# Performance work log

Measured on AMD Instinct MI355X. Metric: run time of the kernel, lower is better.

The kernel has to match this reference:

```python
import jax, jax.numpy as jnp
import numpy as np

K = 16  # neighbors

def _pdist2(a, b):
    # squared euclidean distances (B,N,M); same argsort order as torch.cdist
    return (jnp.sum(a * a, -1)[:, :, None] + jnp.sum(b * b, -1)[:, None, :]
            - 2.0 * jnp.einsum('bnd,bmd->bnm', a, b))

def _knn(xyz, k):
    d2 = jax.lax.stop_gradient(_pdist2(xyz, xyz))
    return jax.lax.top_k(-d2, k)[1]  # (B,N,k) smallest distances

_gather_f = jax.vmap(lambda f, i: f[:, i])  # feat (C,N), idx (...,) -> (C,...)
_gather_x = jax.vmap(lambda x, i: x[i])     # xyz (N,D), idx (...,) -> (...,D)

def _bn_act(x, g, b):
    # eval-mode BatchNorm (running_mean=0, running_var=1) folded to affine, + LeakyReLU(0.1)
    shp = (1, -1) + (1,) * (x.ndim - 2)
    return jax.nn.leaky_relu(x * g.reshape(shp) + b.reshape(shp), 0.1)

def _lfa(xyz, feat, idx, Wm, gm, bm, Ws, Wp, gp, bp):
    # xyz (B,N,3), feat (B,C,N), idx (B,N,K)
    neigh_feat = _gather_f(feat, idx)          # (B,C,N,K)
    neigh_xyz = _gather_x(xyz, idx)            # (B,N,K,3)
    center = xyz[:, :, None, :]
    diff = center - neigh_xyz
    dist = jnp.linalg.norm(diff, axis=-1, keepdims=True)
    rel = jnp.concatenate([diff, dist, jnp.broadcast_to(center, neigh_xyz.shape), neigh_xyz], axis=-1)
    rel = jnp.transpose(rel, (0, 3, 1, 2))     # (B,10,N,K)
    x = jnp.concatenate([neigh_feat, rel], axis=1)          # (B,C+10,N,K)
    x = _bn_act(jnp.einsum('oc,bcnk->bonk', Wm, x), gm, bm)  # (B,O,N,K)
    a = jax.nn.softmax(jnp.einsum('oc,bcnk->bonk', Ws, x), axis=3)
    x = jnp.sum(x * a, axis=3)                               # attentive pool over K -> (B,O,N)
    return _bn_act(jnp.einsum('oc,bcn->bon', Wp, x), gp, bp)

def _interp(src_xyz, src_feat, tgt_xyz):
    nn_idx = jnp.argmin(jax.lax.stop_gradient(_pdist2(tgt_xyz, src_xyz)), axis=-1)  # (B,N)
    return _gather_f(src_feat, nn_idx)  # (B,C,N)


def setup_inputs() -> dict:
    key = jax.random.key(0)
    ks = jax.random.split(key, 24)
    B, N, CIN, NC = 2, 8192, 6, 13
    M1, M2 = N // 2, N // 4
    w = lambda i, shp: jax.random.normal(ks[i], shp, jnp.float32) * 0.05
    ones = lambda c: jnp.ones((c,), jnp.float32)
    zeros = lambda c: jnp.zeros((c,), jnp.float32)
    inp = {
        'xyz': jax.random.uniform(ks[0], (B, N, 3), jnp.float32),
        'feat': jax.random.normal(ks[1], (B, N, CIN), jnp.float32),
        'sel1': jax.random.randint(ks[2], (B, M1), 0, N),
        'sel2': jax.random.randint(ks[3], (B, M2), 0, M1),
        'Wpre': w(4, (64, CIN)), 'gpre': ones(64), 'bpre': zeros(64),
        'W1m': w(5, (64, 74)), 'g1m': ones(64), 'b1m': zeros(64),
        'W1s': w(6, (64, 64)), 'W1p': w(7, (64, 64)), 'g1p': ones(64), 'b1p': zeros(64),
        'W2m': w(8, (128, 74)), 'g2m': ones(128), 'b2m': zeros(128),
        'W2s': w(9, (128, 128)), 'W2p': w(10, (128, 128)), 'g2p': ones(128), 'b2p': zeros(128),
        'W3m': w(11, (256, 138)), 'g3m': ones(256), 'b3m': zeros(256),
        'W3s': w(12, (256, 256)), 'W3p': w(13, (256, 256)), 'g3p': ones(256), 'b3p': zeros(256),
        'Wu2': w(14, (128, 384)), 'gu2': ones(128), 'bu2': zeros(128),
        'Wu1': w(15, (64, 192)), 'gu1': ones(64), 'bu1': zeros(64),
        'Wh1': w(16, (64, 64)), 'bh1': zeros(64),
        'Wh2': w(17, (NC, 64)), 'bh2': zeros(NC),
    }
    return inp


def reference(xyz, feat, sel1, sel2, Wpre, gpre, bpre,
              W1m, g1m, b1m, W1s, W1p, g1p, b1p,
              W2m, g2m, b2m, W2s, W2p, g2p, b2p,
              W3m, g3m, b3m, W3s, W3p, g3p, b3p,
              Wu2, gu2, bu2, Wu1, gu1, bu1,
              Wh1, bh1, Wh2, bh2):
    ft = jnp.transpose(feat, (0, 2, 1))                       # (B,Cin,N)
    x0 = _bn_act(jnp.einsum('oc,bcn->bon', Wpre, ft), gpre, bpre)
    n0 = _knn(xyz, K)
    x1 = _lfa(xyz, x0, n0, W1m, g1m, b1m, W1s, W1p, g1p, b1p)  # (B,64,N)
    xyz1 = _gather_x(xyz, sel1); f1 = _gather_f(x1, sel1)      # random downsample 0.5
    n1 = _knn(xyz1, K)
    x2 = _lfa(xyz1, f1, n1, W2m, g2m, b2m, W2s, W2p, g2p, b2p)  # (B,128,M1)
    xyz2 = _gather_x(xyz1, sel2); f2 = _gather_f(x2, sel2)
    n2 = _knn(xyz2, K)
    x3 = _lfa(xyz2, f2, n2, W3m, g3m, b3m, W3s, W3p, g3p, b3p)  # (B,256,M2)
    up2 = _interp(xyz2, x3, xyz1)
    d2 = _bn_act(jnp.einsum('oc,bcn->bon', Wu2, jnp.concatenate([up2, x2], 1)), gu2, bu2)
    up1 = _interp(xyz1, d2, xyz)
    d1 = _bn_act(jnp.einsum('oc,bcn->bon', Wu1, jnp.concatenate([up1, x1], 1)), gu1, bu1)
    h = jax.nn.leaky_relu(jnp.einsum('oc,bcn->bon', Wh1, d1) + bh1[None, :, None], 0.1)
    logits = jnp.einsum('oc,bcn->bon', Wh2, h) + bh2[None, :, None]
    return jnp.transpose(logits, (0, 2, 1))                    # (B,N,num_classes)
```

## Files before the change

kernel.cpp:

```cpp
#include <hip/hip_runtime.h>
#include <hip/hip_bf16.h>

#pragma clang fp contract(off)

typedef unsigned long long ull;

__device__ __forceinline__ float lrelu(float v) { return v >= 0.0f ? v : 0.1f * v; }

__device__ __forceinline__ float sumsq3(float x, float y, float z) {
    return ((x * x) + (y * y)) + (z * z);
}

__device__ __forceinline__ float dot3fma(float ax, float ay, float az,
                                         float bx, float by, float bz) {
    float d = ax * bx;
    d = __builtin_fmaf(ay, by, d);
    d = __builtin_fmaf(az, bz, d);
    return d;
}

__device__ __forceinline__ float distf(float qn, float sn, float dot) {
    float s = qn + sn;
    return __builtin_fmaf(-2.0f, dot, s);
}

__device__ __forceinline__ ull packkey(float d, int i) {
    unsigned u = __float_as_uint(d);
    u = (u & 0x80000000u) ? ~u : (u | 0x80000000u);
    return ((ull)u << 32) | (unsigned)i;
}

__device__ __forceinline__ ull shfl_xor_u64(ull v, int mask) {
    int lo = __shfl_xor((int)(v & 0xffffffffull), mask);
    int hi = __shfl_xor((int)(v >> 32), mask);
    return ((ull)(unsigned)hi << 32) | (unsigned)lo;
}

__device__ __forceinline__ void cswap64(ull& x, ull& y) {
    bool sw = y < x;
    ull lo = sw ? y : x;
    ull hi = sw ? x : y;
    x = lo; y = hi;
}

__device__ __forceinline__ ull min64(ull a, ull b) { return a < b ? a : b; }

__global__ void k_pre(const float* __restrict__ feat, const float* __restrict__ W,
                      const float* __restrict__ g, const float* __restrict__ bb,
                      float* __restrict__ x0) {
    int p = blockIdx.x * blockDim.x + threadIdx.x;
    if (p >= 2 * 8192) return;
    const float* f = feat + (size_t)p * 6;
    float fv[6];
#pragma unroll
    for (int c = 0; c < 6; ++c) fv[c] = f[c];
    float* out = x0 + (size_t)p * 64;
    for (int o = 0; o < 64; ++o) {
        float s = 0.0f;
#pragma unroll
        for (int c = 0; c < 6; ++c) s = __builtin_fmaf(W[o * 6 + c], fv[c], s);
        float v = s * g[o];
        v = v + bb[o];
        out[o] = lrelu(v);
    }
}

__global__ void k_wt(const float* __restrict__ W, float* __restrict__ WT, int M, int K) {
    int i = blockIdx.x * 256 + threadIdx.x;
    if (i >= M * K) return;
    int o = i / K, c = i - o * K;
    WT[c * M + o] = W[i];
}

template <int LPQ, int TS>
__launch_bounds__(256)
__global__ void k_knn_reg(const float* __restrict__ xyz, int* __restrict__ out_idx, int Npts) {
    constexpr int QPB = 256 / LPQ;
    __shared__ float4 sp[TS];
    int b = blockIdx.y;
    int tid = threadIdx.x;
    int qi = tid / LPQ;
    int l = tid % LPQ;
    int q = blockIdx.x * QPB + qi;
    const float* X = xyz + (size_t)b * Npts * 3;
    float qx = X[q * 3], qy = X[q * 3 + 1], qz = X[q * 3 + 2];
    float qn = sumsq3(qx, qy, qz);

    ull key[16];
#pragma unroll
    for (int u = 0; u < 16; ++u) key[u] = ~0ull;
    ull p0 = ~0ull, p1 = ~0ull, p2 = ~0ull, p3 = ~0ull;
    int cnt = 0;
    float tau_d = INFINITY;

    auto merge = [&]() {
        cswap64(p0, p2); cswap64(p1, p3); cswap64(p0, p1);
        cswap64(p2, p3); cswap64(p1, p2);
        key[12] = min64(key[12], p3);
        key[13] = min64(key[13], p2);
        key[14] = min64(key[14], p1);
        key[15] = min64(key[15], p0);
#pragma unroll
        for (int dstep = 8; dstep >= 1; dstep >>= 1) {
#pragma unroll
            for (int i = 0; i < 16; ++i) {
                if (!(i & dstep)) cswap64(key[i], key[i + dstep]);
            }
        }
        p0 = p1 = p2 = p3 = ~0ull;
        cnt = 0;
        ull t = key[15];
#pragma unroll
        for (int mask = 1; mask < LPQ; mask <<= 1) t = min64(t, shfl_xor_u64(t, mask));
        unsigned hu = (unsigned)(t >> 32);
        unsigned fb = (hu & 0x80000000u) ? (hu & 0x7fffffffu) : ~hu;
        tau_d = (hu == 0xffffffffu) ? INFINITY : __uint_as_float(fb);
    };

    for (int t0 = 0; t0 < Npts; t0 += TS) {
        __syncthreads();
        for (int j = tid; j < TS; j += 256) {
            int i = t0 + j;
            float px = X[i * 3], py = X[i * 3 + 1], pz = X[i * 3 + 2];
            sp[j] = make_float4(px, py, pz, sumsq3(px, py, pz));
        }
        __syncthreads();
        for (int j = l; j < TS; j += LPQ) {
            float4 p = sp[j];
            float d = distf(qn, p.w, dot3fma(qx, qy, qz, p.x, p.y, p.z));
            if (d <= tau_d) {
                p3 = p2; p2 = p1; p1 = p0;
                p0 = packkey(d, t0 + j);
                ++cnt;
            }
            if (__any(cnt >= 4)) merge();
        }
    }
    if (__any(cnt > 0)) merge();

    for (int mask = 1; mask < LPQ; mask <<= 1) {
        ull ok[16];
#pragma unroll
        for (int i = 0; i < 16; ++i) ok[i] = shfl_xor_u64(key[15 - i], mask);
#pragma unroll
        for (int i = 0; i < 16; ++i) key[i] = min64(ok[i], key[i]);
#pragma unroll
        for (int dstep = 8; dstep >= 1; dstep >>= 1) {
#pragma unroll
            for (int i = 0; i < 16; ++i) {
                if (!(i & dstep)) cswap64(key[i], key[i + dstep]);
            }
        }
    }

    if (l == 0) {
        int* o = out_idx + ((size_t)b * Npts + q) * 16;
#pragma unroll
        for (int u = 0; u < 16; ++u) o[u] = (int)(unsigned)(key[u] & 0xffffffffull);
    }
}

template <int C>
__global__ void k_gather(const float* __restrict__ src_xyz, const float* __restrict__ src_feat,
                         const int* __restrict__ sel, float* __restrict__ dst_xyz,
                         float* __restrict__ dst_feat, int M, int Nsrc) {
    int b = blockIdx.y, m = blockIdx.x;
    int s = sel[(size_t)b * M + m];
    const float* fx = src_xyz + ((size_t)b * Nsrc + s) * 3;
    const float* ff = src_feat + ((size_t)b * Nsrc + s) * C;
    float* dx = dst_xyz + ((size_t)b * M + m) * 3;
    float* df = dst_feat + ((size_t)b * M + m) * C;
    if (threadIdx.x < 3) dx[threadIdx.x] = fx[threadIdx.x];
    for (int c = threadIdx.x; c < C; c += blockDim.x) df[c] = ff[c];
}

template <int CIN, int COUT, int NCOL>
__launch_bounds__(256)
__global__ void k_lfa(const float* __restrict__ xyz, const float* __restrict__ feat,
                      const int* __restrict__ kn,
                      const float* __restrict__ WmT, const float* __restrict__ gm, const float* __restrict__ bm,
                      const float* __restrict__ WsT,
                      const float* __restrict__ WpT, const float* __restrict__ gp, const float* __restrict__ bp,
                      float* __restrict__ outf, int Npts) {
    constexpr int CR = CIN + 10;
    constexpr int PPB = NCOL / 16;
    constexpr int RT = COUT / 16;
    constexpr int CT = NCOL / 16;
    constexpr int TPG = 16 / CT;
    constexpr int BUFR = (CR > COUT) ? CR : COUT;
    static_assert(CR % 2 == 0 && COUT % 2 == 0 && CT % 4 == 0 && RT % 4 == 0, "geom");
    __shared__ __align__(16) float buf[BUFR * NCOL];
    int b = blockIdx.y, tid = threadIdx.x;
    int n0 = blockIdx.x * PPB;
    const float* X = xyz + (size_t)b * Npts * 3;

    {
        constexpr int TPC = 256 / NCOL;
        int jl = tid % NCOL;
        int cp = tid / NCOL;
        int n = n0 + (jl >> 4);
        int k = jl & 15;
        int nbr = kn[((size_t)b * Npts + n) * 16 + k];
        const float* fr = feat + ((size_t)b * Npts + nbr) * CIN;
        for (int c = cp; c < CIN; c += TPC) buf[c * NCOL + jl] = fr[c];
        if (cp == 0) {
            float cx = X[n * 3], cy = X[n * 3 + 1], cz = X[n * 3 + 2];
            float nx = X[nbr * 3], ny = X[nbr * 3 + 1], nz = X[nbr * 3 + 2];
            float dx = cx - nx, dy = cy - ny, dz = cz - nz;
            float dn = sqrtf(sumsq3(dx, dy, dz));
            buf[(CIN + 0) * NCOL + jl] = dx; buf[(CIN + 1) * NCOL + jl] = dy;
            buf[(CIN + 2) * NCOL + jl] = dz; buf[(CIN + 3) * NCOL + jl] = dn;
            buf[(CIN + 4) * NCOL + jl] = cx; buf[(CIN + 5) * NCOL + jl] = cy;
            buf[(CIN + 6) * NCOL + jl] = cz; buf[(CIN + 7) * NCOL + jl] = nx;
            buf[(CIN + 8) * NCOL + jl] = ny; buf[(CIN + 9) * NCOL + jl] = nz;
        }
    }
    __syncthreads();

    int tx = tid & 15, ty = tid >> 4;
    float acc[RT][CT];

    auto loadA = [&](float* a, const float* WT, int c) {
#pragma unroll
        for (int r4 = 0; r4 < RT; r4 += 4)
            *reinterpret_cast<float4*>(&a[r4]) =
                *reinterpret_cast<const float4*>(&WT[c * COUT + ty * RT + r4]);
    };
    auto loadB = [&](float* bv, int c) {
#pragma unroll
        for (int c4 = 0; c4 < CT; c4 += 4)
            *reinterpret_cast<float4*>(&bv[c4]) =
                *reinterpret_cast<const float4*>(&buf[c * NCOL + tx * CT + c4]);
    };

#pragma unroll
    for (int r = 0; r < RT; ++r)
#pragma unroll
        for (int cc = 0; cc < CT; ++cc) acc[r][cc] = 0.0f;
    {
        float aA[RT], bvA[CT], aB[RT], bvB[CT];
        loadA(aA, WmT, 0); loadB(bvA, 0);
        for (int c = 0; c < CR; c += 2) {
            loadA(aB, WmT, c + 1); loadB(bvB, c + 1);
#pragma unroll
            for (int r = 0; r < RT; ++r)
#pragma unroll
                for (int cc = 0; cc < CT; ++cc)
                    acc[r][cc] = __builtin_fmaf(aA[r], bvA[cc], acc[r][cc]);
            if (c + 2 < CR) { loadA(aA, WmT, c + 2); loadB(bvA, c + 2); }
#pragma unroll
            for (int r = 0; r < RT; ++r)
#pragma unroll
                for (int cc = 0; cc < CT; ++cc)
                    acc[r][cc] = __builtin_fmaf(aB[r], bvB[cc], acc[r][cc]);
        }
    }
    __syncthreads();
#pragma unroll
    for (int r = 0; r < RT; ++r) {
        int o = ty * RT + r;
        float gg = gm[o], bbv = bm[o];
        float vv[CT];
#pragma unroll
        for (int cc = 0; cc < CT; ++cc) {
            float v = acc[r][cc] * gg;
            v = v + bbv;
            vv[cc] = lrelu(v);
        }
#pragma unroll
        for (int c4 = 0; c4 < CT; c4 += 4)
            *reinterpret_cast<float4*>(&buf[o * NCOL + tx * CT + c4]) =
                *reinterpret_cast<const float4*>(&vv[c4]);
    }
    __syncthreads();

#pragma unroll
    for (int r = 0; r < RT; ++r)
#pragma unroll
        for (int cc = 0; cc < CT; ++cc) acc[r][cc] = 0.0f;
    {
        float aA[RT], bvA[CT], aB[RT], bvB[CT];
        loadA(aA, WsT, 0); loadB(bvA, 0);
        for (int c = 0; c < COUT; c += 2) {
            loadA(aB, WsT, c + 1); loadB(bvB, c + 1);
#pragma unroll
            for (int r = 0; r < RT; ++r)
#pragma unroll
                for (int cc = 0; cc < CT; ++cc)
                    acc[r][cc] = __builtin_fmaf(aA[r], bvA[cc], acc[r][cc]);
            if (c + 2 < COUT) { loadA(aA, WsT, c + 2); loadB(bvA, c + 2); }
#pragma unroll
            for (int r = 0; r < RT; ++r)
#pragma unroll
                for (int cc = 0; cc < CT; ++cc)
                    acc[r][cc] = __builtin_fmaf(aB[r], bvB[cc], acc[r][cc]);
        }
    }
    float pwv[RT];
#pragma unroll
    for (int r = 0; r < RT; ++r) {
        int o = ty * RT + r;
        float m = acc[r][0];
#pragma unroll
        for (int cc = 1; cc < CT; ++cc) m = fmaxf(m, acc[r][cc]);
#pragma unroll
        for (int mask = 1; mask < TPG; mask <<= 1) m = fmaxf(m, __shfl_xor(m, mask));
        float e[CT]; float ps = 0.0f;
#pragma unroll
        for (int cc = 0; cc < CT; ++cc) { e[cc] = expf(acc[r][cc] - m); ps = ps + e[cc]; }
        float tot = ps;
#pragma unroll
        for (int mask = 1; mask < TPG; mask <<= 1) tot = tot + __shfl_xor(tot, mask);
        float xm[CT];
#pragma unroll
        for (int c4 = 0; c4 < CT; c4 += 4)
            *reinterpret_cast<float4*>(&xm[c4]) =
                *reinterpret_cast<const float4*>(&buf[o * NCOL + tx * CT + c4]);
        float pw = 0.0f;
#pragma unroll
        for (int cc = 0; cc < CT; ++cc) {
            float a_ = e[cc] / tot;
            float t = xm[cc] * a_;
            pw = pw + t;
        }
#pragma unroll
        for (int mask = 1; mask < TPG; mask <<= 1) pw = pw + __shfl_xor(pw, mask);
        pwv[r] = pw;
    }
    __syncthreads();
    if (tx % TPG == 0) {
        int pt = tx / TPG;
#pragma unroll
        for (int r = 0; r < RT; ++r) buf[(ty * RT + r) * PPB + pt] = pwv[r];
    }
    __syncthreads();

    constexpr int NOUT = (COUT * PPB) / 256;
    constexpr int PSTEP = 256 / COUT;
    int o = tid % COUT;
    int pbase = tid / COUT;
    float sacc[NOUT];
#pragma unroll
    for (int u = 0; u < NOUT; ++u) sacc[u] = 0.0f;
#pragma unroll 4
    for (int c = 0; c < COUT; ++c) {
        float wv = WpT[c * COUT + o];
#pragma unroll
        for (int u = 0; u < NOUT; ++u)
            sacc[u] = __builtin_fmaf(wv, buf[c * PPB + pbase + u * PSTEP], sacc[u]);
    }
    float gg = gp[o], bbv = bp[o];
#pragma unroll
    for (int u = 0; u < NOUT; ++u) {
        float v = sacc[u] * gg;
        v = v + bbv;
        int p = pbase + u * PSTEP;
        outf[((size_t)b * Npts + n0 + p) * COUT + o] = lrelu(v);
    }
}

template <int LPQ, int TS>
__launch_bounds__(256)
__global__ void k_nn_par(const float* __restrict__ tgt, const float* __restrict__ src,
                         int* __restrict__ nn, int Mt, int Ms) {
    constexpr int QPB = 256 / LPQ;
    __shared__ float4 sp[TS];
    int b = blockIdx.y;
    int tid = threadIdx.x;
    int qi = tid / LPQ;
    int l = tid % LPQ;
    int q = blockIdx.x * QPB + qi;
    const float* T = tgt + (size_t)b * Mt * 3;
    const float* S = src + (size_t)b * Ms * 3;
    float qx = T[q * 3], qy = T[q * 3 + 1], qz = T[q * 3 + 2];
    float qn = sumsq3(qx, qy, qz);
    float bd = INFINITY; int bi = 0x7fffffff;
    for (int t0 = 0; t0 < Ms; t0 += TS) {
        __syncthreads();
        for (int j = tid; j < TS; j += 256) {
            int i = t0 + j;
            float px = S[i * 3], py = S[i * 3 + 1], pz = S[i * 3 + 2];
            sp[j] = make_float4(px, py, pz, sumsq3(px, py, pz));
        }
        __syncthreads();
        for (int j = l; j < TS; j += LPQ) {
            float4 p = sp[j];
            float d = distf(qn, p.w, dot3fma(qx, qy, qz, p.x, p.y, p.z));
            if (d < bd) { bd = d; bi = t0 + j; }
        }
    }
#pragma unroll
    for (int s = LPQ / 2; s; s >>= 1) {
        float od = __shfl_xor(bd, s);
        int oi = __shfl_xor(bi, s);
        bool better = (od < bd) || ((od == bd) && (oi < bi));
        bd = better ? od : bd;
        bi = better ? oi : bi;
    }
    if (l == 0) nn[(size_t)b * Mt + q] = bi;
}

template <int CSRC, int CSKIP, int COUT>
__global__ void k_up(const float* __restrict__ srcf, const float* __restrict__ skipf,
                     const int* __restrict__ nn,
                     const float* __restrict__ W, const float* __restrict__ g, const float* __restrict__ bb,
                     float* __restrict__ outf, int Mt, int Ms) {
    __shared__ float fin[CSRC + CSKIP];
    int b = blockIdx.y, n = blockIdx.x, tid = threadIdx.x;
    int j = nn[(size_t)b * Mt + n];
    const float* fs = srcf + ((size_t)b * Ms + j) * CSRC;
    const float* fk = skipf + ((size_t)b * Mt + n) * CSKIP;
    for (int c = tid; c < CSRC; c += blockDim.x) fin[c] = fs[c];
    for (int c = tid; c < CSKIP; c += blockDim.x) fin[CSRC + c] = fk[c];
    __syncthreads();
    for (int o = tid; o < COUT; o += blockDim.x) {
        const float* wr = W + (size_t)o * (CSRC + CSKIP);
        float s = 0.0f;
        for (int c = 0; c < CSRC + CSKIP; ++c) s = __builtin_fmaf(wr[c], fin[c], s);
        float v = s * g[o]; v = v + bb[o];
        outf[((size_t)b * Mt + n) * COUT + o] = lrelu(v);
    }
}

__global__ void k_u1head(const float* __restrict__ srcf, const float* __restrict__ skipf,
                         const int* __restrict__ nn,
                         const float* __restrict__ Wu1, const float* __restrict__ gu1, const float* __restrict__ bu1,
                         const float* __restrict__ Wh1, const float* __restrict__ bh1,
                         const float* __restrict__ Wh2, const float* __restrict__ bh2,
                         float* __restrict__ out, int Mt, int Ms) {
    __shared__ float fin[192];
    __shared__ float d1[64];
    __shared__ float h[64];
    int b = blockIdx.y, n = blockIdx.x, tid = threadIdx.x;
    int j = nn[(size_t)b * Mt + n];
    const float* fs = srcf + ((size_t)b * Ms + j) * 128;
    const float* fk = skipf + ((size_t)b * Mt + n) * 64;
    for (int c = tid; c < 128; c += 64) fin[c] = fs[c];
    fin[128 + tid] = fk[tid];
    __syncthreads();
    {
        const float* wr = Wu1 + (size_t)tid * 192;
        float s = 0.0f;
        for (int c = 0; c < 192; ++c) s = __builtin_fmaf(wr[c], fin[c], s);
        float v = s * gu1[tid]; v = v + bu1[tid];
        d1[tid] = lrelu(v);
    }
    __syncthreads();
    {
        const float* wr = Wh1 + (size_t)tid * 64;
        float s = 0.0f;
        for (int c = 0; c < 64; ++c) s = __builtin_fmaf(wr[c], d1[c], s);
        float v = s + bh1[tid];
        h[tid] = lrelu(v);
    }
    __syncthreads();
    if (tid < 13) {
        const float* wr = Wh2 + (size_t)tid * 64;
        float s = 0.0f;
        for (int c = 0; c < 64; ++c) s = __builtin_fmaf(wr[c], h[c], s);
        out[((size_t)b * Mt + n) * 13 + tid] = s + bh2[tid];
    }
}

extern "C" void kernel_launch(void* const* d_in, const int* in_sizes, int n_in,
                              void* d_out, int out_size, void* d_ws, size_t ws_size,
                              hipStream_t stream) {
    const float* xyz  = (const float*)d_in[0];
    const float* feat = (const float*)d_in[1];
    const int*   sel1 = (const int*)d_in[2];
    const int*   sel2 = (const int*)d_in[3];
    const float* Wpre = (const float*)d_in[4];
    const float* gpre = (const float*)d_in[5];
    const float* bpre = (const float*)d_in[6];
    const float* W1m  = (const float*)d_in[7];
    const float* g1m  = (const float*)d_in[8];
    const float* b1m  = (const float*)d_in[9];
    const float* W1s  = (const float*)d_in[10];
    const float* W1p  = (const float*)d_in[11];
    const float* g1p  = (const float*)d_in[12];
    const float* b1p  = (const float*)d_in[13];
    const float* W2m  = (const float*)d_in[14];
    const float* g2m  = (const float*)d_in[15];
    const float* b2m  = (const float*)d_in[16];
    const float* W2s  = (const float*)d_in[17];
    const float* W2p  = (const float*)d_in[18];
    const float* g2p  = (const float*)d_in[19];
    const float* b2p  = (const float*)d_in[20];
    const float* W3m  = (const float*)d_in[21];
    const float* g3m  = (const float*)d_in[22];
    const float* b3m  = (const float*)d_in[23];
    const float* W3s  = (const float*)d_in[24];
    const float* W3p  = (const float*)d_in[25];
    const float* g3p  = (const float*)d_in[26];
    const float* b3p  = (const float*)d_in[27];
    const float* Wu2  = (const float*)d_in[28];
    const float* gu2  = (const float*)d_in[29];
    const float* bu2  = (const float*)d_in[30];
    const float* Wu1  = (const float*)d_in[31];
    const float* gu1  = (const float*)d_in[32];
    const float* bu1  = (const float*)d_in[33];
    const float* Wh1  = (const float*)d_in[34];
    const float* bh1  = (const float*)d_in[35];
    const float* Wh2  = (const float*)d_in[36];
    const float* bh2  = (const float*)d_in[37];
    float* out = (float*)d_out;

    char* w = (char*)d_ws;
    auto alloc = [&](size_t n) { char* p = w; w += (n + 255) & ~(size_t)255; return p; };
    float* x0   = (float*)alloc((size_t)2 * 8192 * 64 * 4);
    float* x1   = (float*)alloc((size_t)2 * 8192 * 64 * 4);
    float* f1   = (float*)alloc((size_t)2 * 4096 * 64 * 4);
    float* x2   = (float*)alloc((size_t)2 * 4096 * 128 * 4);
    float* f2   = (float*)alloc((size_t)2 * 2048 * 128 * 4);
    float* x3   = (float*)alloc((size_t)2 * 2048 * 256 * 4);
    float* d2f  = (float*)alloc((size_t)2 * 4096 * 128 * 4);
    float* xyz1 = (float*)alloc((size_t)2 * 4096 * 3 * 4);
    float* xyz2 = (float*)alloc((size_t)2 * 2048 * 3 * 4);
    int* n0   = (int*)alloc((size_t)2 * 8192 * 16 * 4);
    int* n1   = (int*)alloc((size_t)2 * 4096 * 16 * 4);
    int* n2   = (int*)alloc((size_t)2 * 2048 * 16 * 4);
    int* nnu2 = (int*)alloc((size_t)2 * 4096 * 4);
    int* nnu1 = (int*)alloc((size_t)2 * 8192 * 4);
    float* WmT1 = (float*)alloc((size_t)74 * 64 * 4);
    float* WsT1 = (float*)alloc((size_t)64 * 64 * 4);
    float* WpT1 = (float*)alloc((size_t)64 * 64 * 4);
    float* WmT2 = (float*)alloc((size_t)74 * 128 * 4);
    float* WsT2 = (float*)alloc((size_t)128 * 128 * 4);
    float* WpT2 = (float*)alloc((size_t)128 * 128 * 4);
    float* WmT3 = (float*)alloc((size_t)138 * 256 * 4);
    float* WsT3 = (float*)alloc((size_t)256 * 256 * 4);
    float* WpT3 = (float*)alloc((size_t)256 * 256 * 4);

    k_pre<<<128, 128, 0, stream>>>(feat, Wpre, gpre, bpre, x0);
    k_wt<<<(64 * 74 + 255) / 256, 256, 0, stream>>>(W1m, WmT1, 64, 74);
    k_wt<<<(64 * 64 + 255) / 256, 256, 0, stream>>>(W1s, WsT1, 64, 64);
    k_wt<<<(64 * 64 + 255) / 256, 256, 0, stream>>>(W1p, WpT1, 64, 64);
    k_wt<<<(128 * 74 + 255) / 256, 256, 0, stream>>>(W2m, WmT2, 128, 74);
    k_wt<<<(128 * 128 + 255) / 256, 256, 0, stream>>>(W2s, WsT2, 128, 128);
    k_wt<<<(128 * 128 + 255) / 256, 256, 0, stream>>>(W2p, WpT2, 128, 128);
    k_wt<<<(256 * 138 + 255) / 256, 256, 0, stream>>>(W3m, WmT3, 256, 138);
    k_wt<<<(256 * 256 + 255) / 256, 256, 0, stream>>>(W3s, WsT3, 256, 256);
    k_wt<<<(256 * 256 + 255) / 256, 256, 0, stream>>>(W3p, WpT3, 256, 256);

    k_knn_reg<32, 1024><<<dim3(1024, 2), 256, 0, stream>>>(xyz, n0, 8192);
    k_lfa<64, 64, 128><<<dim3(8192 / 8, 2), 256, 0, stream>>>(
        xyz, x0, n0, WmT1, g1m, b1m, WsT1, WpT1, g1p, b1p, x1, 8192);

    k_gather<64><<<dim3(4096, 2), 64, 0, stream>>>(xyz, x1, sel1, xyz1, f1, 4096, 8192);
    k_knn_reg<32, 1024><<<dim3(512, 2), 256, 0, stream>>>(xyz1, n1, 4096);
    k_lfa<64, 128, 128><<<dim3(4096 / 8, 2), 256, 0, stream>>>(
        xyz1, f1, n1, WmT2, g2m, b2m, WsT2, WpT2, g2p, b2p, x2, 4096);

    k_gather<128><<<dim3(2048, 2), 64, 0, stream>>>(xyz1, x2, sel2, xyz2, f2, 2048, 4096);
    k_knn_reg<32, 1024><<<dim3(256, 2), 256, 0, stream>>>(xyz2, n2, 2048);
    k_lfa<128, 256, 64><<<dim3(2048 / 4, 2), 256, 0, stream>>>(
        xyz2, f2, n2, WmT3, g3m, b3m, WsT3, WpT3, g3p, b3p, x3, 2048);

    k_nn_par<16, 512><<<dim3(256, 2), 256, 0, stream>>>(xyz1, xyz2, nnu2, 4096, 2048);
    k_up<256, 128, 128><<<dim3(4096, 2), 128, 0, stream>>>(x3, x2, nnu2, Wu2, gu2, bu2,
                                                           d2f, 4096, 2048);
    k_nn_par<16, 512><<<dim3(512, 2), 256, 0, stream>>>(xyz, xyz1, nnu1, 8192, 4096);
    k_u1head<<<dim3(8192, 2), 64, 0, stream>>>(d2f, x1, nnu1, Wu1, gu1, bu1, Wh1, bh1,
                                               Wh2, bh2, out, 8192, 4096);
}
```

Baseline: 1.198 ms.

## Batch points per block in upsample/head, widen LFA blocks, fuse weight transposes

Merges the nine weight-transpose launches into one 2D-grid kernel. The LFA kernel gets a thread-count template parameter: stages 2 and 3 now run with 512 threads, so each thread holds fewer accumulator rows, and the double-buffered operand prefetch is replaced by a simple loop. The upsample and head kernels now handle four points per block, so each weight load is reused across four points instead of being re-read for every point. The trade-offs are fewer blocks per launch, lost explicit prefetch overlap in the LFA inner loops, and the shared-memory and register behaviour of the wider blocks.

```diff
diff --git a/kernel.cpp b/kernel.cpp
--- a/kernel.cpp
+++ b/kernel.cpp
@@ -65,11 +65,26 @@
     }
 }
 
-__global__ void k_wt(const float* __restrict__ W, float* __restrict__ WT, int M, int K) {
+__global__ void k_wt_all(const float* __restrict__ s0, const float* __restrict__ s1,
+                         const float* __restrict__ s2, const float* __restrict__ s3,
+                         const float* __restrict__ s4, const float* __restrict__ s5,
+                         const float* __restrict__ s6, const float* __restrict__ s7,
+                         const float* __restrict__ s8,
+                         float* __restrict__ d0, float* __restrict__ d1,
+                         float* __restrict__ d2, float* __restrict__ d3,
+                         float* __restrict__ d4, float* __restrict__ d5,
+                         float* __restrict__ d6, float* __restrict__ d7,
+                         float* __restrict__ d8) {
+    const int Ms[9] = {64, 64, 64, 128, 128, 128, 256, 256, 256};
+    const int Ks[9] = {74, 64, 64, 74, 128, 128, 138, 256, 256};
+    const float* S[9] = {s0, s1, s2, s3, s4, s5, s6, s7, s8};
+    float* D[9] = {d0, d1, d2, d3, d4, d5, d6, d7, d8};
+    int seg = blockIdx.y;
+    int M = Ms[seg], K = Ks[seg];
     int i = blockIdx.x * 256 + threadIdx.x;
     if (i >= M * K) return;
     int o = i / K, c = i - o * K;
-    WT[c * M + o] = W[i];
+    D[seg][c * M + o] = S[seg][i];
 }
 
 template <int LPQ, int TS>
@@ -174,8 +189,8 @@
     for (int c = threadIdx.x; c < C; c += blockDim.x) df[c] = ff[c];
 }
 
-template <int CIN, int COUT, int NCOL>
-__launch_bounds__(256)
+template <int CIN, int COUT, int NCOL, int THREADS>
+__launch_bounds__(THREADS)
 __global__ void k_lfa(const float* __restrict__ xyz, const float* __restrict__ feat,
                       const int* __restrict__ kn,
                       const float* __restrict__ WmT, const float* __restrict__ gm, const float* __restrict__ bm,
@@ -184,18 +199,19 @@
                       float* __restrict__ outf, int Npts) {
     constexpr int CR = CIN + 10;
     constexpr int PPB = NCOL / 16;
-    constexpr int RT = COUT / 16;
+    constexpr int BANDS = THREADS / 16;
+    constexpr int RT = COUT / BANDS;
     constexpr int CT = NCOL / 16;
     constexpr int TPG = 16 / CT;
     constexpr int BUFR = (CR > COUT) ? CR : COUT;
-    static_assert(CR % 2 == 0 && COUT % 2 == 0 && CT % 4 == 0 && RT % 4 == 0, "geom");
+    static_assert(RT % 4 == 0 && CT % 4 == 0, "geom");
     __shared__ __align__(16) float buf[BUFR * NCOL];
     int b = blockIdx.y, tid = threadIdx.x;
     int n0 = blockIdx.x * PPB;
     const float* X = xyz + (size_t)b * Npts * 3;
 
     {
-        constexpr int TPC = 256 / NCOL;
+        constexpr int TPC = THREADS / NCOL;
         int jl = tid % NCOL;
         int cp = tid / NCOL;
         int n = n0 + (jl >> 4);
@@ -237,23 +253,14 @@
     for (int r = 0; r < RT; ++r)
 #pragma unroll
         for (int cc = 0; cc < CT; ++cc) acc[r][cc] = 0.0f;
-    {
-        float aA[RT], bvA[CT], aB[RT], bvB[CT];
-        loadA(aA, WmT, 0); loadB(bvA, 0);
-        for (int c = 0; c < CR; c += 2) {
-            loadA(aB, WmT, c + 1); loadB(bvB, c + 1);
-#pragma unroll
-            for (int r = 0; r < RT; ++r)
-#pragma unroll
-                for (int cc = 0; cc < CT; ++cc)
-                    acc[r][cc] = __builtin_fmaf(aA[r], bvA[cc], acc[r][cc]);
-            if (c + 2 < CR) { loadA(aA, WmT, c + 2); loadB(bvA, c + 2); }
-#pragma unroll
-            for (int r = 0; r < RT; ++r)
-#pragma unroll
-                for (int cc = 0; cc < CT; ++cc)
-                    acc[r][cc] = __builtin_fmaf(aB[r], bvB[cc], acc[r][cc]);
-        }
+    for (int c = 0; c < CR; ++c) {
+        float a[RT], bv[CT];
+        loadA(a, WmT, c); loadB(bv, c);
+#pragma unroll
+        for (int r = 0; r < RT; ++r)
+#pragma unroll
+            for (int cc = 0; cc < CT; ++cc)
+                acc[r][cc] = __builtin_fmaf(a[r], bv[cc], acc[r][cc]);
     }
     __syncthreads();
 #pragma unroll
@@ -278,23 +285,14 @@
     for (int r = 0; r < RT; ++r)
 #pragma unroll
         for (int cc = 0; cc < CT; ++cc) acc[r][cc] = 0.0f;
-    {
-        float aA[RT], bvA[CT], aB[RT], bvB[CT];
-        loadA(aA, WsT, 0); loadB(bvA, 0);
-        for (int c = 0; c < COUT; c += 2) {
-            loadA(aB, WsT, c + 1); loadB(bvB, c + 1);
-#pragma unroll
-            for (int r = 0; r < RT; ++r)
-#pragma unroll
-                for (int cc = 0; cc < CT; ++cc)
-                    acc[r][cc] = __builtin_fmaf(aA[r], bvA[cc], acc[r][cc]);
-            if (c + 2 < COUT) { loadA(aA, WsT, c + 2); loadB(bvA, c + 2); }
-#pragma unroll
-            for (int r = 0; r < RT; ++r)
-#pragma unroll
-                for (int cc = 0; cc < CT; ++cc)
-                    acc[r][cc] = __builtin_fmaf(aB[r], bvB[cc], acc[r][cc]);
-        }
+    for (int c = 0; c < COUT; ++c) {
+        float a[RT], bv[CT];
+        loadA(a, WsT, c); loadB(bv, c);
+#pragma unroll
+        for (int r = 0; r < RT; ++r)
+#pragma unroll
+            for (int cc = 0; cc < CT; ++cc)
+                acc[r][cc] = __builtin_fmaf(a[r], bv[cc], acc[r][cc]);
     }
     float pwv[RT];
 #pragma unroll
@@ -335,27 +333,30 @@
     }
     __syncthreads();
 
-    constexpr int NOUT = (COUT * PPB) / 256;
-    constexpr int PSTEP = 256 / COUT;
+    constexpr int TPP = THREADS / COUT;
+    constexpr int NOUT = (PPB + TPP - 1) / TPP;
     int o = tid % COUT;
     int pbase = tid / COUT;
     float sacc[NOUT];
 #pragma unroll
     for (int u = 0; u < NOUT; ++u) sacc[u] = 0.0f;
-#pragma unroll 4
     for (int c = 0; c < COUT; ++c) {
         float wv = WpT[c * COUT + o];
 #pragma unroll
-        for (int u = 0; u < NOUT; ++u)
-            sacc[u] = __builtin_fmaf(wv, buf[c * PPB + pbase + u * PSTEP], sacc[u]);
+        for (int u = 0; u < NOUT; ++u) {
+            int p = pbase + u * TPP;
+            if (p < PPB) sacc[u] = __builtin_fmaf(wv, buf[c * PPB + p], sacc[u]);
+        }
     }
     float gg = gp[o], bbv = bp[o];
 #pragma unroll
     for (int u = 0; u < NOUT; ++u) {
-        float v = sacc[u] * gg;
-        v = v + bbv;
-        int p = pbase + u * PSTEP;
-        outf[((size_t)b * Npts + n0 + p) * COUT + o] = lrelu(v);
+        int p = pbase + u * TPP;
+        if (p < PPB) {
+            float v = sacc[u] * gg;
+            v = v + bbv;
+            outf[((size_t)b * Npts + n0 + p) * COUT + o] = lrelu(v);
+        }
     }
 }
 
@@ -400,25 +401,42 @@
     if (l == 0) nn[(size_t)b * Mt + q] = bi;
 }
 
-template <int CSRC, int CSKIP, int COUT>
+template <int CSRC, int CSKIP, int COUT, int PTS>
 __global__ void k_up(const float* __restrict__ srcf, const float* __restrict__ skipf,
                      const int* __restrict__ nn,
                      const float* __restrict__ W, const float* __restrict__ g, const float* __restrict__ bb,
                      float* __restrict__ outf, int Mt, int Ms) {
-    __shared__ float fin[CSRC + CSKIP];
-    int b = blockIdx.y, n = blockIdx.x, tid = threadIdx.x;
-    int j = nn[(size_t)b * Mt + n];
-    const float* fs = srcf + ((size_t)b * Ms + j) * CSRC;
-    const float* fk = skipf + ((size_t)b * Mt + n) * CSKIP;
-    for (int c = tid; c < CSRC; c += blockDim.x) fin[c] = fs[c];
-    for (int c = tid; c < CSKIP; c += blockDim.x) fin[CSRC + c] = fk[c];
-    __syncthreads();
-    for (int o = tid; o < COUT; o += blockDim.x) {
-        const float* wr = W + (size_t)o * (CSRC + CSKIP);
-        float s = 0.0f;
-        for (int c = 0; c < CSRC + CSKIP; ++c) s = __builtin_fmaf(wr[c], fin[c], s);
-        float v = s * g[o]; v = v + bb[o];
-        outf[((size_t)b * Mt + n) * COUT + o] = lrelu(v);
+    constexpr int CTOT = CSRC + CSKIP;
+    __shared__ float fin[PTS][CTOT];
+    int b = blockIdx.y, tid = threadIdx.x;
+    int n0 = blockIdx.x * PTS;
+#pragma unroll
+    for (int pp = 0; pp < PTS; ++pp) {
+        int n = n0 + pp;
+        int j = nn[(size_t)b * Mt + n];
+        const float* fs = srcf + ((size_t)b * Ms + j) * CSRC;
+        const float* fk = skipf + ((size_t)b * Mt + n) * CSKIP;
+        for (int c = tid; c < CSRC; c += COUT) fin[pp][c] = fs[c];
+        for (int c = tid; c < CSKIP; c += COUT) fin[pp][CSRC + c] = fk[c];
+    }
+    __syncthreads();
+    int o = tid;
+    const float* wr = W + (size_t)o * CTOT;
+    float s[PTS];
+#pragma unroll
+    for (int pp = 0; pp < PTS; ++pp) s[pp] = 0.0f;
+    for (int c = 0; c < CTOT; ++c) {
+        float wv = wr[c];
+#pragma unroll
+        for (int pp = 0; pp < PTS; ++pp)
+            s[pp] = __builtin_fmaf(wv, fin[pp][c], s[pp]);
+    }
+    float gg = g[o], bbv = bb[o];
+#pragma unroll
+    for (int pp = 0; pp < PTS; ++pp) {
+        float v = s[pp] * gg;
+        v = v + bbv;
+        outf[((size_t)b * Mt + n0 + pp) * COUT + o] = lrelu(v);
     }
 }
 
@@ -428,37 +446,69 @@
                          const float* __restrict__ Wh1, const float* __restrict__ bh1,
                          const float* __restrict__ Wh2, const float* __restrict__ bh2,
                          float* __restrict__ out, int Mt, int Ms) {
-    __shared__ float fin[192];
-    __shared__ float d1[64];
-    __shared__ float h[64];
-    int b = blockIdx.y, n = blockIdx.x, tid = threadIdx.x;
-    int j = nn[(size_t)b * Mt + n];
-    const float* fs = srcf + ((size_t)b * Ms + j) * 128;
-    const float* fk = skipf + ((size_t)b * Mt + n) * 64;
-    for (int c = tid; c < 128; c += 64) fin[c] = fs[c];
-    fin[128 + tid] = fk[tid];
+    __shared__ float fin[4][192];
+    __shared__ float d1[4][64];
+    __shared__ float h[4][64];
+    int b = blockIdx.y, tid = threadIdx.x;
+    int n0 = blockIdx.x * 4;
+#pragma unroll
+    for (int pp = 0; pp < 4; ++pp) {
+        int n = n0 + pp;
+        int j = nn[(size_t)b * Mt + n];
+        const float* fs = srcf + ((size_t)b * Ms + j) * 128;
+        const float* fk = skipf + ((size_t)b * Mt + n) * 64;
+        for (int c = tid; c < 128; c += 64) fin[pp][c] = fs[c];
+        fin[pp][128 + tid] = fk[tid];
+    }
     __syncthreads();
     {
         const float* wr = Wu1 + (size_t)tid * 192;
-        float s = 0.0f;
-        for (int c = 0; c < 192; ++c) s = __builtin_fmaf(wr[c], fin[c], s);
-        float v = s * gu1[tid]; v = v + bu1[tid];
-        d1[tid] = lrelu(v);
+        float s[4] = {0.0f, 0.0f, 0.0f, 0.0f};
+        for (int c = 0; c < 192; ++c) {
+            float wv = wr[c];
+#pragma unroll
+            for (int pp = 0; pp < 4; ++pp)
+                s[pp] = __builtin_fmaf(wv, fin[pp][c], s[pp]);
+        }
+        float gg = gu1[tid], bbv = bu1[tid];
+#pragma unroll
+        for (int pp = 0; pp < 4; ++pp) {
+            float v = s[pp] * gg;
+            v = v + bbv;
+            d1[pp][tid] = lrelu(v);
+        }
     }
     __syncthreads();
     {
         const float* wr = Wh1 + (size_t)tid * 64;
-        float s = 0.0f;
-        for (int c = 0; c < 64; ++c) s = __builtin_fmaf(wr[c], d1[c], s);
-        float v = s + bh1[tid];
-        h[tid] = lrelu(v);
+        float s[4] = {0.0f, 0.0f, 0.0f, 0.0f};
+        for (int c = 0; c < 64; ++c) {
+            float wv = wr[c];
+#pragma unroll
+            for (int pp = 0; pp < 4; ++pp)
+                s[pp] = __builtin_fmaf(wv, d1[pp][c], s[pp]);
+        }
+        float bbv = bh1[tid];
+#pragma unroll
+        for (int pp = 0; pp < 4; ++pp) {
+            float v = s[pp] + bbv;
+            h[pp][tid] = lrelu(v);
+        }
     }
     __syncthreads();
     if (tid < 13) {
         const float* wr = Wh2 + (size_t)tid * 64;
-        float s = 0.0f;
-        for (int c = 0; c < 64; ++c) s = __builtin_fmaf(wr[c], h[c], s);
-        out[((size_t)b * Mt + n) * 13 + tid] = s + bh2[tid];
+        float s[4] = {0.0f, 0.0f, 0.0f, 0.0f};
+        for (int c = 0; c < 64; ++c) {
+            float wv = wr[c];
+#pragma unroll
+            for (int pp = 0; pp < 4; ++pp)
+                s[pp] = __builtin_fmaf(wv, h[pp][c], s[pp]);
+        }
+        float bbv = bh2[tid];
+#pragma unroll
+        for (int pp = 0; pp < 4; ++pp)
+            out[((size_t)b * Mt + n0 + pp) * 13 + tid] = s[pp] + bbv;
     }
 }
 
@@ -532,34 +582,28 @@
     float* WpT3 = (float*)alloc((size_t)256 * 256 * 4);
 
     k_pre<<<128, 128, 0, stream>>>(feat, Wpre, gpre, bpre, x0);
-    k_wt<<<(64 * 74 + 255) / 256, 256, 0, stream>>>(W1m, WmT1, 64, 74);
-    k_wt<<<(64 * 64 + 255) / 256, 256, 0, stream>>>(W1s, WsT1, 64, 64);
-    k_wt<<<(64 * 64 + 255) / 256, 256, 0, stream>>>(W1p, WpT1, 64, 64);
-    k_wt<<<(128 * 74 + 255) / 256, 256, 0, stream>>>(W2m, WmT2, 128, 74);
-    k_wt<<<(128 * 128 + 255) / 256, 256, 0, stream>>>(W2s, WsT2, 128, 128);
-    k_wt<<<(128 * 128 + 255) / 256, 256, 0, stream>>>(W2p, WpT2, 128, 128);
-    k_wt<<<(256 * 138 + 255) / 256, 256, 0, stream>>>(W3m, WmT3, 256, 138);
-    k_wt<<<(256 * 256 + 255) / 256, 256, 0, stream>>>(W3s, WsT3, 256, 256);
-    k_wt<<<(256 * 256 + 255) / 256, 256, 0, stream>>>(W3p, WpT3, 256, 256);
+    k_wt_all<<<dim3(256, 9), 256, 0, stream>>>(W1m, W1s, W1p, W2m, W2s, W2p, W3m, W3s, W3p,
+                                               WmT1, WsT1, WpT1, WmT2, WsT2, WpT2,
+                                               WmT3, WsT3, WpT3);
 
     k_knn_reg<32, 1024><<<dim3(1024, 2), 256, 0, stream>>>(xyz, n0, 8192);
-    k_lfa<64, 64, 128><<<dim3(8192 / 8, 2), 256, 0, stream>>>(
+    k_lfa<64, 64, 128, 256><<<dim3(8192 / 8, 2), 256, 0, stream>>>(
         xyz, x0, n0, WmT1, g1m, b1m, WsT1, WpT1, g1p, b1p, x1, 8192);
 
     k_gather<64><<<dim3(4096, 2), 64, 0, stream>>>(xyz, x1, sel1, xyz1, f1, 4096, 8192);
     k_knn_reg<32, 1024><<<dim3(512, 2), 256, 0, stream>>>(xyz1, n1, 4096);
-    k_lfa<64, 128, 128><<<dim3(4096 / 8, 2), 256, 0, stream>>>(
+    k_lfa<64, 128, 128, 512><<<dim3(4096 / 8, 2), 512, 0, stream>>>(
         xyz1, f1, n1, WmT2, g2m, b2m, WsT2, WpT2, g2p, b2p, x2, 4096);
 
     k_gather<128><<<dim3(2048, 2), 64, 0, stream>>>(xyz1, x2, sel2, xyz2, f2, 2048, 4096);
     k_knn_reg<32, 1024><<<dim3(256, 2), 256, 0, stream>>>(xyz2, n2, 2048);
-    k_lfa<128, 256, 64><<<dim3(2048 / 4, 2), 256, 0, stream>>>(
+    k_lfa<128, 256, 64, 512><<<dim3(2048 / 4, 2), 512, 0, stream>>>(
         xyz2, f2, n2, WmT3, g3m, b3m, WsT3, WpT3, g3p, b3p, x3, 2048);
 
     k_nn_par<16, 512><<<dim3(256, 2), 256, 0, stream>>>(xyz1, xyz2, nnu2, 4096, 2048);
-    k_up<256, 128, 128><<<dim3(4096, 2), 128, 0, stream>>>(x3, x2, nnu2, Wu2, gu2, bu2,
-                                                           d2f, 4096, 2048);
+    k_up<256, 128, 128, 4><<<dim3(1024, 2), 128, 0, stream>>>(x3, x2, nnu2, Wu2, gu2, bu2,
+                                                              d2f, 4096, 2048);
     k_nn_par<16, 512><<<dim3(512, 2), 256, 0, stream>>>(xyz, xyz1, nnu1, 8192, 4096);
-    k_u1head<<<dim3(8192, 2), 64, 0, stream>>>(d2f, x1, nnu1, Wu1, gu1, bu1, Wh1, bh1,
+    k_u1head<<<dim3(2048, 2), 64, 0, stream>>>(d2f, x1, nnu1, Wu1, gu1, bu1, Wh1, bh1,
                                                Wh2, bh2, out, 8192, 4096);
 }
```

New measurement: 1.053 ms (median of 2 runs). 12.1% less time.
